# Performance work log

Measured on AMD Instinct MI355X. Metric: run time of the kernel, lower is better.

Reference implementation:

```python
import jax, jax.numpy as jnp
import numpy as np

D_MODEL = 1024
D_FF = 4 * D_MODEL
NUM_EXPERTS = 8
TOP_K = 2


def setup_inputs() -> dict:
    key = jax.random.key(0)
    ks = jax.random.split(key, 7)
    B, S = 2, 2048
    x = jax.random.normal(ks[0], (B, S, D_MODEL), dtype=jnp.float32)
    s = 0.02
    Wr = jax.random.normal(ks[1], (D_MODEL, NUM_EXPERTS), dtype=jnp.float32) * s
    br = jnp.zeros((NUM_EXPERTS,), dtype=jnp.float32)
    W1 = jax.random.normal(ks[2], (NUM_EXPERTS, D_MODEL, D_FF), dtype=jnp.float32) * s
    b1 = jnp.zeros((NUM_EXPERTS, D_FF), dtype=jnp.float32)
    W2 = jax.random.normal(ks[3], (NUM_EXPERTS, D_FF, D_MODEL), dtype=jnp.float32) * s
    b2 = jnp.zeros((NUM_EXPERTS, D_MODEL), dtype=jnp.float32)
    return {"x": x, "Wr": Wr, "br": br, "W1": W1, "b1": b1, "W2": W2, "b2": b2}


def reference(x, Wr, br, W1, b1, W2, b2):
    E, K = NUM_EXPERTS, TOP_K
    # Router: softmax over experts, hard top-k gating, renormalize.
    gate_logits = jnp.einsum('bsd,de->bse', x, Wr) + br  # [B,S,E]
    gate_probs = jax.nn.softmax(gate_logits, axis=-1)
    topk_vals, topk_idx = jax.lax.top_k(gate_probs, K)  # [B,S,K]
    oh = jax.nn.one_hot(topk_idx, E, dtype=gate_probs.dtype)  # [B,S,K,E]
    hard = jnp.einsum('bske,bsk->bse', oh, topk_vals)  # scattered top-k probs
    hard = hard / jnp.clip(hard.sum(axis=-1, keepdims=True), 1e-9)
    # Dense per-expert FFN (every expert sees all tokens, as in the source).
    h = jnp.einsum('bsd,edh->ebsh', x, W1) + b1[:, None, None, :]  # [E,B,S,4D]
    h = jax.nn.gelu(h, approximate=False)  # torch nn.GELU default = exact erf
    y = jnp.einsum('ebsh,ehd->ebsd', h, W2) + b2[:, None, None, :]  # [E,B,S,D]
    output = jnp.einsum('ebsd,bse->bsd', y, hard)
    # Aux load-balancing loss (no mask branch).
    flat_probs = gate_probs.reshape(-1, E)
    assignments = jnp.argmax(flat_probs, axis=-1)
    f = jnp.mean(jax.nn.one_hot(assignments, E, dtype=flat_probs.dtype), axis=0)
    P = flat_probs.mean(axis=0)
    aux_loss = E * jnp.sum(f * P)
    return output, aux_loss
```

## Files before the change

kernel.cpp:

```cpp
#include <hip/hip_runtime.h>
#include <cstdint>
#include <cstddef>

#define NTOK 4096
#define DM   1024
#define DFF  4096
#define NE   8
#define MAXTILES 72

typedef __attribute__((ext_vector_type(8))) __bf16 bf16x8;
typedef __attribute__((ext_vector_type(4))) float  f32x4;

__device__ __forceinline__ unsigned short f2bf(float f) {
  union { float f; unsigned int u; } c; c.f = f;
  unsigned int u = c.u;
  return (unsigned short)((u + 0x7fffu + ((u >> 16) & 1u)) >> 16);
}

__device__ __forceinline__ void async16(const void* g, void* l) {
  __builtin_amdgcn_global_load_lds(
      (const __attribute__((address_space(1))) void*)(uintptr_t)g,
      (__attribute__((address_space(3))) void*)(uint32_t)(uintptr_t)l,
      16, 0, 0);
}

__global__ void k_cvt_x(const float* __restrict__ x, unsigned short* __restrict__ xb) {
  int i = (blockIdx.x * 256 + threadIdx.x) * 4;
  float4 v = *(const float4*)(x + i);
  ushort4 o;
  o.x = f2bf(v.x); o.y = f2bf(v.y); o.z = f2bf(v.z); o.w = f2bf(v.w);
  *(ushort4*)(xb + i) = o;
}

__global__ void k_transpose_bf(const float* __restrict__ src, unsigned short* __restrict__ dst,
                               int R, int C) {
  __shared__ float tile[32][33];
  int e = blockIdx.z;
  src += (size_t)e * R * C;
  dst += (size_t)e * R * C;
  int tx = threadIdx.x, ty = threadIdx.y;
  int c = blockIdx.x * 32 + tx;
#pragma unroll
  for (int q = 0; q < 4; q++) {
    int r = blockIdx.y * 32 + q * 8 + ty;
    tile[q * 8 + ty][tx] = src[(size_t)r * C + c];
  }
  __syncthreads();
#pragma unroll
  for (int q = 0; q < 4; q++) {
    dst[(size_t)(blockIdx.x * 32 + q * 8 + ty) * R + blockIdx.y * 32 + tx] =
        f2bf(tile[tx][q * 8 + ty]);
  }
}

__global__ void k_router(const float* __restrict__ x, const float* __restrict__ Wr,
                         const float* __restrict__ br, int* __restrict__ cnt,
                         int* __restrict__ fcnt, float* __restrict__ Psum,
                         int* __restrict__ toklist, float* __restrict__ wlist) {
  __shared__ float sP[NE];
  __shared__ int sF[NE];
  int tid = threadIdx.x;
  if (tid < NE) { sP[tid] = 0.f; sF[tid] = 0; }
  __syncthreads();
  int tok = blockIdx.x * 32 + (tid >> 3);
  int e = tid & 7;
  const float* xr = x + (size_t)tok * DM;
  float acc = 0.f;
#pragma unroll 4
  for (int i = 0; i < DM; i += 4) {
    float4 xv = *(const float4*)(xr + i);
    acc = fmaf(xv.x, Wr[(i + 0) * NE + e], acc);
    acc = fmaf(xv.y, Wr[(i + 1) * NE + e], acc);
    acc = fmaf(xv.z, Wr[(i + 2) * NE + e], acc);
    acc = fmaf(xv.w, Wr[(i + 3) * NE + e], acc);
  }
  acc += br[e];
  float m = acc;
  for (int s = 1; s < 8; s <<= 1) m = fmaxf(m, __shfl_xor(m, s));
  float p = expf(acc - m);
  float sum = p;
  for (int s = 1; s < 8; s <<= 1) sum += __shfl_xor(sum, s);
  float prob = p / sum;
  atomicAdd(&sP[e], prob);
  int lanebase = (tid & 63) & ~7;
  float pv[8];
#pragma unroll
  for (int j = 0; j < 8; j++) pv[j] = __shfl(prob, lanebase + j);
  if (e == 0) {
    int i1 = 0; float v1 = pv[0];
#pragma unroll
    for (int j = 1; j < 8; j++) if (pv[j] > v1) { v1 = pv[j]; i1 = j; }
    int i2 = -1; float v2 = -1.f;
#pragma unroll
    for (int j = 0; j < 8; j++) if (j != i1 && pv[j] > v2) { v2 = pv[j]; i2 = j; }
    float inv = 1.f / (v1 + v2);
    int s1 = atomicAdd(&cnt[i1], 1);
    toklist[i1 * NTOK + s1] = tok; wlist[i1 * NTOK + s1] = v1 * inv;
    int s2 = atomicAdd(&cnt[i2], 1);
    toklist[i2 * NTOK + s2] = tok; wlist[i2 * NTOK + s2] = v2 * inv;
    atomicAdd(&sF[i1], 1);
  }
  __syncthreads();
  if (tid < NE) { atomicAdd(&Psum[tid], sP[tid]); atomicAdd(&fcnt[tid], sF[tid]); }
}

__global__ void k_scan_aux(const int* __restrict__ cnt, const int* __restrict__ fcnt,
                           const float* __restrict__ Psum, int* __restrict__ offs,
                           int* __restrict__ ntiles, int* __restrict__ tileE,
                           int* __restrict__ tileM0, float* __restrict__ aux_out) {
  if (threadIdx.x == 0) {
    int o = 0; float a = 0.f; int t = 0;
    for (int e = 0; e < NE; e++) {
      offs[e] = o; o += cnt[e];
      a += (float)fcnt[e] * Psum[e];
      for (int m0 = 0; m0 < cnt[e]; m0 += 128) { tileE[t] = e; tileM0[t] = m0; t++; }
    }
    *ntiles = t;
    aux_out[0] = 8.f * a / (4096.f * 4096.f);
  }
}

__global__ __launch_bounds__(256) void k_ffn1(
    const unsigned short* __restrict__ xb, const unsigned short* __restrict__ w1t,
    const float* __restrict__ b1, const int* __restrict__ cnt,
    const int* __restrict__ offs, const int* __restrict__ ntiles,
    const int* __restrict__ tileE, const int* __restrict__ tileM0,
    const int* __restrict__ toklist, unsigned short* __restrict__ H) {
  int t = blockIdx.x;
  if (t >= *ntiles) return;
  int e = tileE[t], m0 = tileM0[t];
  int cn = cnt[e];
  int n0 = blockIdx.y * 128;
  __shared__ __align__(16) unsigned short At[128 * 64];
  __shared__ __align__(16) unsigned short Bt[128 * 64];
  int tid = threadIdx.x;
  int chunk = tid & 7, rsub = tid >> 3;
  int cg = (chunk ^ (rsub & 7)) * 8;
  const unsigned short* gA[4]; const unsigned short* gB[4];
  unsigned short* lA[4]; unsigned short* lB[4];
#pragma unroll
  for (int q = 0; q < 4; q++) {
    int row = q * 32 + rsub;
    int tr = m0 + row; if (tr >= cn) tr = cn - 1;
    int tok = toklist[e * NTOK + tr];
    gA[q] = xb + (size_t)tok * DM + cg;
    gB[q] = w1t + ((size_t)e * DFF + n0 + row) * DM + cg;
    lA[q] = At + row * 64 + chunk * 8;
    lB[q] = Bt + row * 64 + chunk * 8;
  }
  int wid = tid >> 6, lane = tid & 63;
  int mW = (wid >> 1) * 64, nW = (wid & 1) * 64;
  int lr = lane & 15, quad = lane >> 4;
  int sw = lane & 7;
  f32x4 acc[4][4];
#pragma unroll
  for (int i = 0; i < 4; i++)
#pragma unroll
    for (int j = 0; j < 4; j++) acc[i][j] = (f32x4)(0.f);
  for (int k0 = 0; k0 < DM; k0 += 64) {
#pragma unroll
    for (int q = 0; q < 4; q++) async16(gA[q] + k0, lA[q]);
#pragma unroll
    for (int q = 0; q < 4; q++) async16(gB[q] + k0, lB[q]);
    __syncthreads();
#pragma unroll
    for (int kk8 = 0; kk8 < 8; kk8 += 4) {
      int cs = ((kk8 + quad) ^ sw) * 8;
      bf16x8 a[4], b[4];
#pragma unroll
      for (int i = 0; i < 4; i++) a[i] = *(const bf16x8*)(At + (mW + i * 16 + lr) * 64 + cs);
#pragma unroll
      for (int j = 0; j < 4; j++) b[j] = *(const bf16x8*)(Bt + (nW + j * 16 + lr) * 64 + cs);
#pragma unroll
      for (int i = 0; i < 4; i++)
#pragma unroll
        for (int j = 0; j < 4; j++)
          acc[i][j] = __builtin_amdgcn_mfma_f32_16x16x32_bf16(a[i], b[j], acc[i][j], 0, 0, 0);
    }
    __syncthreads();
  }
  int off = offs[e];
#pragma unroll
  for (int i = 0; i < 4; i++) {
#pragma unroll
    for (int r = 0; r < 4; r++) {
      int gr = m0 + mW + i * 16 + quad * 4 + r;
      if (gr < cn) {
        size_t base = (size_t)(off + gr) * DFF + n0;
#pragma unroll
        for (int j = 0; j < 4; j++) {
          int col = nW + j * 16 + lr;
          float v = acc[i][j][r] + b1[(size_t)e * DFF + n0 + col];
          float g = 0.5f * v * (1.f + erff(v * 0.70710678f));
          H[base + col] = f2bf(g);
        }
      }
    }
  }
}

__global__ __launch_bounds__(256) void k_ffn2(
    const unsigned short* __restrict__ H, const unsigned short* __restrict__ w2t,
    const float* __restrict__ b2, const int* __restrict__ cnt,
    const int* __restrict__ offs, const int* __restrict__ ntiles,
    const int* __restrict__ tileE, const int* __restrict__ tileM0,
    const int* __restrict__ toklist, const float* __restrict__ wlist,
    float* __restrict__ out) {
  int t = blockIdx.x;
  if (t >= *ntiles) return;
  int e = tileE[t], m0 = tileM0[t];
  int cn = cnt[e];
  int n0 = blockIdx.y * 128;
  int kz = blockIdx.z;
  int off = offs[e];
  __shared__ __align__(16) unsigned short At[128 * 64];
  __shared__ __align__(16) unsigned short Bt[128 * 64];
  int tid = threadIdx.x;
  int chunk = tid & 7, rsub = tid >> 3;
  int cg = (chunk ^ (rsub & 7)) * 8;
  const unsigned short* gA[4]; const unsigned short* gB[4];
  unsigned short* lA[4]; unsigned short* lB[4];
#pragma unroll
  for (int q = 0; q < 4; q++) {
    int row = q * 32 + rsub;
    int hr = m0 + row; if (hr >= cn) hr = cn - 1;
    gA[q] = H + (size_t)(off + hr) * DFF + cg;
    gB[q] = w2t + ((size_t)e * DM + n0 + row) * DFF + cg;
    lA[q] = At + row * 64 + chunk * 8;
    lB[q] = Bt + row * 64 + chunk * 8;
  }
  int wid = tid >> 6, lane = tid & 63;
  int mW = (wid >> 1) * 64, nW = (wid & 1) * 64;
  int lr = lane & 15, quad = lane >> 4;
  int sw = lane & 7;
  f32x4 acc[4][4];
#pragma unroll
  for (int i = 0; i < 4; i++)
#pragma unroll
    for (int j = 0; j < 4; j++) acc[i][j] = (f32x4)(0.f);
  int kbeg = kz * (DFF / 2), kend = kbeg + DFF / 2;
  for (int k0 = kbeg; k0 < kend; k0 += 64) {
#pragma unroll
    for (int q = 0; q < 4; q++) async16(gA[q] + k0, lA[q]);
#pragma unroll
    for (int q = 0; q < 4; q++) async16(gB[q] + k0, lB[q]);
    __syncthreads();
#pragma unroll
    for (int kk8 = 0; kk8 < 8; kk8 += 4) {
      int cs = ((kk8 + quad) ^ sw) * 8;
      bf16x8 a[4], b[4];
#pragma unroll
      for (int i = 0; i < 4; i++) a[i] = *(const bf16x8*)(At + (mW + i * 16 + lr) * 64 + cs);
#pragma unroll
      for (int j = 0; j < 4; j++) b[j] = *(const bf16x8*)(Bt + (nW + j * 16 + lr) * 64 + cs);
#pragma unroll
      for (int i = 0; i < 4; i++)
#pragma unroll
        for (int j = 0; j < 4; j++)
          acc[i][j] = __builtin_amdgcn_mfma_f32_16x16x32_bf16(a[i], b[j], acc[i][j], 0, 0, 0);
    }
    __syncthreads();
  }
#pragma unroll
  for (int i = 0; i < 4; i++) {
#pragma unroll
    for (int r = 0; r < 4; r++) {
      int gr = m0 + mW + i * 16 + quad * 4 + r;
      if (gr < cn) {
        int tok = toklist[e * NTOK + gr];
        float w = wlist[e * NTOK + gr];
#pragma unroll
        for (int j = 0; j < 4; j++) {
          int col = n0 + nW + j * 16 + lr;
          float v = acc[i][j][r] + (kz == 0 ? b2[(size_t)e * DM + col] : 0.f);
          atomicAdd(&out[(size_t)tok * DM + col], w * v);
        }
      }
    }
  }
}

__global__ void k_wsfail(float* out, float v) { if (threadIdx.x == 0) out[0] = v; }

extern "C" void kernel_launch(void* const* d_in, const int* in_sizes, int n_in,
                              void* d_out, int out_size, void* d_ws, size_t ws_size,
                              hipStream_t stream) {
  const float* x  = (const float*)d_in[0];
  const float* Wr = (const float*)d_in[1];
  const float* br = (const float*)d_in[2];
  const float* W1 = (const float*)d_in[3];
  const float* b1 = (const float*)d_in[4];
  const float* W2 = (const float*)d_in[5];
  const float* b2 = (const float*)d_in[6];
  float* out = (float*)d_out;
  char* ws = (char*)d_ws;

  const size_t NEED = ((size_t)144 << 20) + (size_t)8192 * DFF * 2;
  if (ws_size < NEED) {
    hipLaunchKernelGGL(k_wsfail, dim3(1), dim3(64), 0, stream, out, (float)ws_size);
    return;
  }
  int* cnt      = (int*)(ws + 0);
  int* fcnt     = (int*)(ws + 64);
  float* Psum   = (float*)(ws + 128);
  int* offs     = (int*)(ws + 192);
  int* ntiles   = (int*)(ws + 256);
  int* tileE    = (int*)(ws + 512);
  int* tileM0   = (int*)(ws + 1024);
  int* toklist  = (int*)(ws + 4096);
  float* wlist  = (float*)(ws + 4096 + 131072);
  unsigned short* xb  = (unsigned short*)(ws + ((size_t)1 << 20));
  unsigned short* w1t = (unsigned short*)(ws + ((size_t)10 << 20));
  unsigned short* w2t = (unsigned short*)(ws + ((size_t)80 << 20));
  unsigned short* Hb  = (unsigned short*)(ws + ((size_t)144 << 20));

  hipMemsetAsync(d_out, 0, (size_t)out_size * sizeof(float), stream);
  hipMemsetAsync(ws, 0, 4096, stream);

  hipLaunchKernelGGL(k_cvt_x, dim3(NTOK * DM / 1024), dim3(256), 0, stream, x, xb);
  hipLaunchKernelGGL(k_transpose_bf, dim3(DFF / 32, DM / 32, NE), dim3(32, 8), 0, stream, W1, w1t, DM, DFF);
  hipLaunchKernelGGL(k_transpose_bf, dim3(DM / 32, DFF / 32, NE), dim3(32, 8), 0, stream, W2, w2t, DFF, DM);
  hipLaunchKernelGGL(k_router, dim3(NTOK / 32), dim3(256), 0, stream, x, Wr, br, cnt, fcnt, Psum, toklist, wlist);
  hipLaunchKernelGGL(k_scan_aux, dim3(1), dim3(64), 0, stream, cnt, fcnt, Psum, offs, ntiles, tileE, tileM0, out + (out_size - 1));
  hipLaunchKernelGGL(k_ffn1, dim3(MAXTILES, DFF / 128), dim3(256), 0, stream,
                     xb, w1t, b1, cnt, offs, ntiles, tileE, tileM0, toklist, Hb);
  hipLaunchKernelGGL(k_ffn2, dim3(MAXTILES, DM / 128, 2), dim3(256), 0, stream,
                     Hb, w2t, b2, cnt, offs, ntiles, tileE, tileM0, toklist, wlist, out);
}
```

Baseline: 741.3 us.

## Replace FFN2 atomic scatter with partial buffers and a per-token combine kernel

FFN2 no longer applies bias and gate weight and atomically adds into the output. Instead it writes per-split-K partial results into a dense buffer placed over the now-dead W1 copy. A new combine kernel then reads each token's two expert rows, adds the bias and writes the weighted sum, using a token-to-slot map recorded by the router. This also removes the output memset. Separately, the GEMM grids are reordered so consecutive blocks share the same token tile, and exact erff is replaced by a polynomial erf approximation. In exchange the change adds an extra kernel and a 64 MB partial-buffer round trip.

```diff
diff --git a/kernel.cpp b/kernel.cpp
--- a/kernel.cpp
+++ b/kernel.cpp
@@ -22,6 +22,21 @@
       (const __attribute__((address_space(1))) void*)(uintptr_t)g,
       (__attribute__((address_space(3))) void*)(uint32_t)(uintptr_t)l,
       16, 0, 0);
+}
+
+__device__ __forceinline__ float gelu_erf(float v) {
+  float u = v * 0.70710678118f;
+  float az = fabsf(u);
+  float t = __builtin_amdgcn_rcpf(fmaf(0.3275911f, az, 1.f));
+  float p = fmaf(1.061405429f, t, -1.453152027f);
+  p = fmaf(p, t, 1.421413741f);
+  p = fmaf(p, t, -0.284496736f);
+  p = fmaf(p, t, 0.254829592f);
+  p = p * t;
+  float ex = __builtin_amdgcn_exp2f(-az * az * 1.44269504089f);
+  float er = fmaf(-p, ex, 1.f);
+  er = copysignf(er, u);
+  return 0.5f * v * (1.f + er);
 }
 
 __global__ void k_cvt_x(const float* __restrict__ x, unsigned short* __restrict__ xb) {
@@ -56,7 +71,8 @@
 __global__ void k_router(const float* __restrict__ x, const float* __restrict__ Wr,
                          const float* __restrict__ br, int* __restrict__ cnt,
                          int* __restrict__ fcnt, float* __restrict__ Psum,
-                         int* __restrict__ toklist, float* __restrict__ wlist) {
+                         int* __restrict__ toklist, float* __restrict__ wlist,
+                         int* __restrict__ tokmap, float* __restrict__ tokw) {
   __shared__ float sP[NE];
   __shared__ int sF[NE];
   int tid = threadIdx.x;
@@ -98,6 +114,8 @@
     toklist[i1 * NTOK + s1] = tok; wlist[i1 * NTOK + s1] = v1 * inv;
     int s2 = atomicAdd(&cnt[i2], 1);
     toklist[i2 * NTOK + s2] = tok; wlist[i2 * NTOK + s2] = v2 * inv;
+    tokmap[tok * 2] = (i1 << 16) | s1;  tokw[tok * 2] = v1 * inv;
+    tokmap[tok * 2 + 1] = (i2 << 16) | s2; tokw[tok * 2 + 1] = v2 * inv;
     atomicAdd(&sF[i1], 1);
   }
   __syncthreads();
@@ -126,11 +144,11 @@
     const int* __restrict__ offs, const int* __restrict__ ntiles,
     const int* __restrict__ tileE, const int* __restrict__ tileM0,
     const int* __restrict__ toklist, unsigned short* __restrict__ H) {
-  int t = blockIdx.x;
+  int t = blockIdx.y;
   if (t >= *ntiles) return;
   int e = tileE[t], m0 = tileM0[t];
   int cn = cnt[e];
-  int n0 = blockIdx.y * 128;
+  int n0 = blockIdx.x * 128;
   __shared__ __align__(16) unsigned short At[128 * 64];
   __shared__ __align__(16) unsigned short Bt[128 * 64];
   int tid = threadIdx.x;
@@ -191,8 +209,7 @@
         for (int j = 0; j < 4; j++) {
           int col = nW + j * 16 + lr;
           float v = acc[i][j][r] + b1[(size_t)e * DFF + n0 + col];
-          float g = 0.5f * v * (1.f + erff(v * 0.70710678f));
-          H[base + col] = f2bf(g);
+          H[base + col] = f2bf(gelu_erf(v));
         }
       }
     }
@@ -201,16 +218,14 @@
 
 __global__ __launch_bounds__(256) void k_ffn2(
     const unsigned short* __restrict__ H, const unsigned short* __restrict__ w2t,
-    const float* __restrict__ b2, const int* __restrict__ cnt,
-    const int* __restrict__ offs, const int* __restrict__ ntiles,
-    const int* __restrict__ tileE, const int* __restrict__ tileM0,
-    const int* __restrict__ toklist, const float* __restrict__ wlist,
-    float* __restrict__ out) {
-  int t = blockIdx.x;
+    const int* __restrict__ cnt, const int* __restrict__ offs,
+    const int* __restrict__ ntiles, const int* __restrict__ tileE,
+    const int* __restrict__ tileM0, float* __restrict__ P) {
+  int t = blockIdx.y;
   if (t >= *ntiles) return;
   int e = tileE[t], m0 = tileM0[t];
   int cn = cnt[e];
-  int n0 = blockIdx.y * 128;
+  int n0 = blockIdx.x * 128;
   int kz = blockIdx.z;
   int off = offs[e];
   __shared__ __align__(16) unsigned short At[128 * 64];
@@ -261,23 +276,49 @@
     }
     __syncthreads();
   }
+  float* Pk = P + (size_t)kz * 8192 * DM;
 #pragma unroll
   for (int i = 0; i < 4; i++) {
 #pragma unroll
     for (int r = 0; r < 4; r++) {
       int gr = m0 + mW + i * 16 + quad * 4 + r;
       if (gr < cn) {
-        int tok = toklist[e * NTOK + gr];
-        float w = wlist[e * NTOK + gr];
+        size_t base = (size_t)(off + gr) * DM + n0;
 #pragma unroll
         for (int j = 0; j < 4; j++) {
-          int col = n0 + nW + j * 16 + lr;
-          float v = acc[i][j][r] + (kz == 0 ? b2[(size_t)e * DM + col] : 0.f);
-          atomicAdd(&out[(size_t)tok * DM + col], w * v);
+          int col = nW + j * 16 + lr;
+          Pk[base + col] = acc[i][j][r];
         }
       }
     }
   }
+}
+
+__global__ __launch_bounds__(256) void k_combine(
+    const float* __restrict__ P, const float* __restrict__ b2,
+    const int* __restrict__ offs, const int* __restrict__ tokmap,
+    const float* __restrict__ tokw, float* __restrict__ out) {
+  int tok = blockIdx.x;
+  int c4 = threadIdx.x * 4;
+  int enc0 = tokmap[tok * 2], enc1 = tokmap[tok * 2 + 1];
+  float w0 = tokw[tok * 2], w1 = tokw[tok * 2 + 1];
+  int e0 = enc0 >> 16, p0 = enc0 & 0xffff;
+  int e1 = enc1 >> 16, p1 = enc1 & 0xffff;
+  size_t r0 = (size_t)(offs[e0] + p0) * DM;
+  size_t r1 = (size_t)(offs[e1] + p1) * DM;
+  const size_t KZ = (size_t)8192 * DM;
+  float4 a0 = *(const float4*)(P + r0 + c4);
+  float4 a1 = *(const float4*)(P + KZ + r0 + c4);
+  float4 c0 = *(const float4*)(P + r1 + c4);
+  float4 c1 = *(const float4*)(P + KZ + r1 + c4);
+  float4 bb0 = *(const float4*)(b2 + (size_t)e0 * DM + c4);
+  float4 bb1 = *(const float4*)(b2 + (size_t)e1 * DM + c4);
+  float4 o;
+  o.x = w0 * (a0.x + a1.x + bb0.x) + w1 * (c0.x + c1.x + bb1.x);
+  o.y = w0 * (a0.y + a1.y + bb0.y) + w1 * (c0.y + c1.y + bb1.y);
+  o.z = w0 * (a0.z + a1.z + bb0.z) + w1 * (c0.z + c1.z + bb1.z);
+  o.w = w0 * (a0.w + a1.w + bb0.w) + w1 * (c0.w + c1.w + bb1.w);
+  *(float4*)(out + (size_t)tok * DM + c4) = o;
 }
 
 __global__ void k_wsfail(float* out, float v) { if (threadIdx.x == 0) out[0] = v; }
@@ -308,22 +349,27 @@
   int* tileE    = (int*)(ws + 512);
   int* tileM0   = (int*)(ws + 1024);
   int* toklist  = (int*)(ws + 4096);
-  float* wlist  = (float*)(ws + 4096 + 131072);
+  float* wlist  = (float*)(ws + 135168);
+  int* tokmap   = (int*)(ws + 266240);
+  float* tokw   = (float*)(ws + 299008);
   unsigned short* xb  = (unsigned short*)(ws + ((size_t)1 << 20));
   unsigned short* w1t = (unsigned short*)(ws + ((size_t)10 << 20));
+  float*          Pp  = (float*)(ws + ((size_t)10 << 20));
   unsigned short* w2t = (unsigned short*)(ws + ((size_t)80 << 20));
   unsigned short* Hb  = (unsigned short*)(ws + ((size_t)144 << 20));
 
-  hipMemsetAsync(d_out, 0, (size_t)out_size * sizeof(float), stream);
   hipMemsetAsync(ws, 0, 4096, stream);
 
   hipLaunchKernelGGL(k_cvt_x, dim3(NTOK * DM / 1024), dim3(256), 0, stream, x, xb);
   hipLaunchKernelGGL(k_transpose_bf, dim3(DFF / 32, DM / 32, NE), dim3(32, 8), 0, stream, W1, w1t, DM, DFF);
   hipLaunchKernelGGL(k_transpose_bf, dim3(DM / 32, DFF / 32, NE), dim3(32, 8), 0, stream, W2, w2t, DFF, DM);
-  hipLaunchKernelGGL(k_router, dim3(NTOK / 32), dim3(256), 0, stream, x, Wr, br, cnt, fcnt, Psum, toklist, wlist);
+  hipLaunchKernelGGL(k_router, dim3(NTOK / 32), dim3(256), 0, stream, x, Wr, br, cnt, fcnt, Psum,
+                     toklist, wlist, tokmap, tokw);
   hipLaunchKernelGGL(k_scan_aux, dim3(1), dim3(64), 0, stream, cnt, fcnt, Psum, offs, ntiles, tileE, tileM0, out + (out_size - 1));
-  hipLaunchKernelGGL(k_ffn1, dim3(MAXTILES, DFF / 128), dim3(256), 0, stream,
+  hipLaunchKernelGGL(k_ffn1, dim3(DFF / 128, MAXTILES), dim3(256), 0, stream,
                      xb, w1t, b1, cnt, offs, ntiles, tileE, tileM0, toklist, Hb);
-  hipLaunchKernelGGL(k_ffn2, dim3(MAXTILES, DM / 128, 2), dim3(256), 0, stream,
-                     Hb, w2t, b2, cnt, offs, ntiles, tileE, tileM0, toklist, wlist, out);
-}
+  hipLaunchKernelGGL(k_ffn2, dim3(DM / 128, MAXTILES, 2), dim3(256), 0, stream,
+                     Hb, w2t, cnt, offs, ntiles, tileE, tileM0, Pp);
+  hipLaunchKernelGGL(k_combine, dim3(NTOK), dim3(256), 0, stream,
+                     Pp, b2, offs, tokmap, tokw, out);
+}
```

New measurement: 652.2 us. 12.0% less time.
